# Performance work log

Hardware: AMD Instinct MI355X
Metric: run time of the kernel (lower is better)

## Reference

```python
import jax, jax.numpy as jnp
import numpy as np

B, L, H, W, C = 8, 512, 768, 12, 25
S = L * W          # span_idx count, reshaped to [B, L, W, H]
Hh = H // 2        # per-direction LSTM hidden (bidirectional)


def setup_inputs() -> dict:
    key = jax.random.key(0)
    ks = jax.random.split(key, 24)
    p = lambda k, shape: jax.random.normal(k, shape, jnp.float32) * 0.02
    z = lambda n: jnp.zeros((n,), jnp.float32)
    return {
        "we": jax.random.normal(ks[0], (B, L, H), jnp.float32),
        "mask": jnp.ones((B, L), jnp.int32),
        "span_idx": jax.random.randint(ks[1], (B, S, 2), 0, L, jnp.int32),
        "pe": jax.random.normal(ks[2], (B, C, H), jnp.float32),
        # BiLSTM params (PyTorch gate order i,f,g,o)
        "w_ih_f": p(ks[3], (4 * Hh, H)), "w_hh_f": p(ks[4], (4 * Hh, Hh)),
        "b_ih_f": z(4 * Hh), "b_hh_f": z(4 * Hh),
        "w_ih_b": p(ks[5], (4 * Hh, H)), "w_hh_b": p(ks[6], (4 * Hh, Hh)),
        "b_ih_b": z(4 * Hh), "b_hh_b": z(4 * Hh),
        # project_start MLP: H -> 4H -> H
        "start_w1": p(ks[7], (4 * H, H)), "start_b1": z(4 * H),
        "start_w2": p(ks[8], (H, 4 * H)), "start_b2": z(H),
        # project_end MLP
        "end_w1": p(ks[9], (4 * H, H)), "end_b1": z(4 * H),
        "end_w2": p(ks[10], (H, 4 * H)), "end_b2": z(H),
        # out_project MLP: 2H -> 4H -> H
        "out_w1": p(ks[11], (4 * H, 2 * H)), "out_b1": z(4 * H),
        "out_w2": p(ks[12], (H, 4 * H)), "out_b2": z(H),
        # prompt_proj MLP: H -> 4H -> H
        "pr_w1": p(ks[13], (4 * H, H)), "pr_b1": z(4 * H),
        "pr_w2": p(ks[14], (H, 4 * H)), "pr_b2": z(H),
    }


def lstm_dir(x, w_ih, w_hh, b_ih, b_hh, reverse):
    # x: [B,L,D] -> per-direction hidden sequence [B,L,Hh]
    xg = jnp.einsum('bld,gd->blg', x, w_ih) + b_ih  # precomputed input gates
    n = w_hh.shape[1]

    def step(carry, xg_t):
        h, c = carry
        g = xg_t + h @ w_hh.T + b_hh
        i, f, gg, o = jnp.split(g, 4, axis=-1)
        c = jax.nn.sigmoid(f) * c + jax.nn.sigmoid(i) * jnp.tanh(gg)
        h = jax.nn.sigmoid(o) * jnp.tanh(c)
        return (h, c), h

    init = (jnp.zeros((x.shape[0], n), x.dtype), jnp.zeros((x.shape[0], n), x.dtype))
    _, hs = jax.lax.scan(step, init, jnp.swapaxes(xg, 0, 1), reverse=reverse)
    return jnp.swapaxes(hs, 0, 1)


def mlp(x, w1, b1, w2, b2):
    # Linear -> ReLU -> (Dropout: identity in eval) -> Linear
    return jax.nn.relu(x @ w1.T + b1) @ w2.T + b2


def extract_elements(t, idx):
    # t: [B,L,D], idx: [B,S] -> [B,S,D]; indices clamped like torch
    idx = jnp.clip(idx, 0, t.shape[1] - 1)
    return jnp.take_along_axis(t, idx[..., None], axis=1)


def reference(we, mask, span_idx, pe,
              w_ih_f, w_hh_f, b_ih_f, b_hh_f,
              w_ih_b, w_hh_b, b_ih_b, b_hh_b,
              start_w1, start_b1, start_w2, start_b2,
              end_w1, end_b1, end_w2, end_b2,
              out_w1, out_b1, out_w2, out_b2,
              pr_w1, pr_b1, pr_w2, pr_b2):
    # 1) Bidirectional LSTM encoder (pad_packed zeros masked positions)
    hf = lstm_dir(we, w_ih_f, w_hh_f, b_ih_f, b_hh_f, reverse=False)
    hb = lstm_dir(we, w_ih_b, w_hh_b, b_ih_b, b_hh_b, reverse=True)
    h = jnp.concatenate([hf, hb], axis=-1) * mask[..., None].astype(we.dtype)
    # 2) SpanMarkerV0: dual MLP -> gather -> concat+relu -> out MLP
    start_rep = mlp(h, start_w1, start_b1, start_w2, start_b2)
    end_rep = mlp(h, end_w1, end_b1, end_w2, end_b2)
    ss = extract_elements(start_rep, span_idx[:, :, 0])
    es = extract_elements(end_rep, span_idx[:, :, 1])
    cat = jax.nn.relu(jnp.concatenate([ss, es], axis=-1))
    span = mlp(cat, out_w1, out_b1, out_w2, out_b2).reshape(B, L, W, H)
    # 3) Prompt projection
    prompt = mlp(pe, pr_w1, pr_b1, pr_w2, pr_b2)
    return (span, prompt)
```

## Files before the change

### kernel.cpp

```cpp
#include <hip/hip_runtime.h>
#include <hip/hip_bf16.h>
#include <stdint.h>

#define B_ 8
#define L_ 512
#define H_ 768
#define WW_ 12
#define C_ 25
#define S_ (L_*WW_)
#define HH 384
#define G4 1536

using bf16x8 = __attribute__((ext_vector_type(8))) short;
using f32x4  = __attribute__((ext_vector_type(4))) float;

static __device__ __forceinline__ unsigned short f2bf(float x){
  unsigned u = __float_as_uint(x);
  unsigned r = (u + 0x7FFFu + ((u >> 16) & 1u)) >> 16;
  return (unsigned short)r;
}
static __device__ __forceinline__ float bflo(unsigned u){ return __uint_as_float(u << 16); }
static __device__ __forceinline__ float bfhi(unsigned u){ return __uint_as_float(u & 0xFFFF0000u); }

static __device__ __forceinline__ float sigmoid_f(float x){
  x = fminf(15.f, fmaxf(-15.f, x));
  return 1.f / (1.f + __expf(-x));
}
static __device__ __forceinline__ float tanh_f(float x){
  x = fminf(15.f, fmaxf(-15.f, x));
  float e = __expf(-2.f * x);
  return (1.f - e) / (1.f + e);
}

static __device__ __forceinline__ void gl_lds16(const unsigned short* g, unsigned short* l){
  __builtin_amdgcn_global_load_lds(
      (const __attribute__((address_space(1))) unsigned int*)g,
      (__attribute__((address_space(3))) unsigned int*)l,
      16, 0, 0);
}

struct CastArgs {
  const float* s[14];
  unsigned short* d[14];
  long cum[15];
};

__global__ __launch_bounds__(256) void k_cast_multi(CastArgs a, long total){
  long i = (long)blockIdx.x * blockDim.x + threadIdx.x;
  if (i >= total) return;
  int seg = 0;
  while (i >= a.cum[seg + 1]) seg++;
  long j = i - a.cum[seg];
  float4 v = reinterpret_cast<const float4*>(a.s[seg])[j];
  ushort4 o;
  o.x = f2bf(v.x); o.y = f2bf(v.y); o.z = f2bf(v.z); o.w = f2bf(v.w);
  reinterpret_cast<ushort4*>(a.d[seg])[j] = o;
}

__global__ void k_biascomb2(const float* __restrict__ bihf, const float* __restrict__ bhhf,
                            const float* __restrict__ bihb, const float* __restrict__ bhhb,
                            float* __restrict__ o){
  int i = blockIdx.x * blockDim.x + threadIdx.x;
  if (i < 1536) o[i] = bihf[i] + bhhf[i];
  else if (i < 3072) o[i] = bihb[i - 1536] + bhhb[i - 1536];
}

template<int ACT, int OUTBF, int GX>
static __device__ __forceinline__ void gemm2_body(
    const unsigned short* __restrict__ A, const unsigned short* __restrict__ Bm,
    const float* __restrict__ bias, void* __restrict__ Cout,
    int M, int N, int K, int lda, int ldb)
{
  __shared__ unsigned short Al[128 * 64];
  __shared__ unsigned short Bl[128 * 64];

  const int tid  = threadIdx.x;
  const int lane = tid & 63;
  const int wave = tid >> 6;
  const int wr = wave >> 1, wc = wave & 1;
  const int l16 = lane & 15, lq = lane >> 4;
  const int m0 = (GX == 0 ? blockIdx.y : blockIdx.x) * 128;
  const int n0 = (GX == 0 ? blockIdx.x : blockIdx.y) * 128;

  const int r_ = tid >> 3;
  const int p_ = tid & 7;
  const int cS = ((p_ ^ (r_ & 7)) * 8);
  const unsigned short* Asrc[4];
  const unsigned short* Bsrc[4];
  #pragma unroll
  for (int i = 0; i < 4; i++){
    int ra = m0 + i * 32 + r_; ra = ra < M ? ra : (M - 1);
    Asrc[i] = A + (size_t)ra * lda + cS;
    int rb = n0 + i * 32 + r_; rb = rb < N ? rb : (N - 1);
    Bsrc[i] = Bm + (size_t)rb * ldb + cS;
  }

  f32x4 acc[4][4];
  #pragma unroll
  for (int a = 0; a < 4; a++)
    #pragma unroll
    for (int b = 0; b < 4; b++)
      acc[a][b] = (f32x4)0.f;

  const int sw0 = ((0 * 4 + lq) ^ (l16 & 7)) * 16;
  const int sw1 = ((1 * 4 + lq) ^ (l16 & 7)) * 16;
  const int aBase = (wr * 64 + l16) * 128;
  const int bBase = (wc * 64 + l16) * 128;

  for (int k0 = 0; k0 < K; k0 += 64){
    #pragma unroll
    for (int i = 0; i < 4; i++)
      gl_lds16(Asrc[i] + k0, Al + i * 2048 + tid * 8);
    #pragma unroll
    for (int i = 0; i < 4; i++)
      gl_lds16(Bsrc[i] + k0, Bl + i * 2048 + tid * 8);
    __syncthreads();

    #pragma unroll
    for (int kk = 0; kk < 2; kk++){
      const int sw = kk ? sw1 : sw0;
      bf16x8 av[4], bv[4];
      #pragma unroll
      for (int mi = 0; mi < 4; mi++)
        av[mi] = *reinterpret_cast<const bf16x8*>((const char*)Al + aBase + mi * 2048 + sw);
      #pragma unroll
      for (int ni = 0; ni < 4; ni++)
        bv[ni] = *reinterpret_cast<const bf16x8*>((const char*)Bl + bBase + ni * 2048 + sw);
      #pragma unroll
      for (int mi = 0; mi < 4; mi++)
        #pragma unroll
        for (int ni = 0; ni < 4; ni++)
          acc[mi][ni] = __builtin_amdgcn_mfma_f32_16x16x32_bf16(av[mi], bv[ni], acc[mi][ni], 0, 0, 0);
    }
    __syncthreads();
  }

  #pragma unroll
  for (int mi = 0; mi < 4; mi++){
    #pragma unroll
    for (int r = 0; r < 4; r++){
      int row = m0 + wr * 64 + mi * 16 + lq * 4 + r;
      if (row >= M) continue;
      #pragma unroll
      for (int ni = 0; ni < 4; ni++){
        int col = n0 + wc * 64 + ni * 16 + l16;
        float v = acc[mi][ni][r] + bias[col];
        if (ACT) v = v > 0.f ? v : 0.f;
        if (OUTBF) ((unsigned short*)Cout)[(size_t)row * N + col] = f2bf(v);
        else       ((float*)Cout)[(size_t)row * N + col] = v;
      }
    }
  }
}

template<int ACT, int OUTBF, int GX = 0>
__global__ __launch_bounds__(256) void k_gemm2(
    const unsigned short* A, const unsigned short* Bm,
    const float* bias, void* Cout, int M, int N, int K, int lda, int ldb)
{
  gemm2_body<ACT, OUTBF, GX>(A, Bm, bias, Cout, M, N, K, lda, ldb);
}

struct GemmPair {
  const unsigned short *A0, *A1, *B0, *B1;
  const float *b0, *b1;
  void *C0, *C1;
};

template<int ACT, int OUTBF, int GX = 0>
__global__ __launch_bounds__(256) void k_gemm2z(
    GemmPair p, int M, int N, int K, int lda, int ldb)
{
  const int z = blockIdx.z;
  gemm2_body<ACT, OUTBF, GX>(z ? p.A1 : p.A0, z ? p.B1 : p.B0,
                             z ? p.b1 : p.b0, z ? p.C1 : p.C0,
                             M, N, K, lda, ldb);
}

__global__ __launch_bounds__(512, 4) void k_gout(
    const unsigned short* __restrict__ Ps, const unsigned short* __restrict__ Pe,
    const int* __restrict__ sidx, const float* __restrict__ b1,
    const unsigned short* __restrict__ Bw, const float* __restrict__ b2,
    float* __restrict__ out)
{
  __shared__ unsigned short Al[128 * 64];
  __shared__ unsigned short Bl[256 * 64];
  __shared__ int idx2[128][2];

  const int tid  = threadIdx.x;
  const int lane = tid & 63;
  const int wave = tid >> 6;
  const int wr = wave >> 2;
  const int wc = wave & 3;
  const int l16 = lane & 15, lq = lane >> 4;

  const int wg   = blockIdx.x;
  const int xcd  = wg & 7;
  const int slot = wg >> 3;
  const int nblk = slot % 3;
  const int tm   = xcd + 8 * (slot / 3);
  const int b  = tm / 48;
  const int s0 = (tm % 48) * 128;
  const int n0 = nblk * 256;

  if (tid < 128){
    int s = s0 + tid;
    int i0 = sidx[((size_t)b * S_ + s) * 2 + 0];
    int i1 = sidx[((size_t)b * S_ + s) * 2 + 1];
    idx2[tid][0] = min(max(i0, 0), L_ - 1);
    idx2[tid][1] = min(max(i1, 0), L_ - 1);
  }
  __syncthreads();

  const int r_ = tid >> 3;
  const int p_ = tid & 7;
  const int cS = ((p_ ^ (r_ & 7)) * 8);
  const unsigned short* Bsrc[4];
  const unsigned short* As0[2];
  const unsigned short* As1[2];
  #pragma unroll
  for (int i = 0; i < 4; i++)
    Bsrc[i] = Bw + (size_t)(n0 + i * 64 + r_) * 3072 + cS;
  #pragma unroll
  for (int i = 0; i < 2; i++){
    int rr = i * 64 + r_;
    As0[i] = Ps + (size_t)(b * L_ + idx2[rr][0]) * 3072 + cS;
    As1[i] = Pe + (size_t)(b * L_ + idx2[rr][1]) * 3072 + cS;
  }

  f32x4 acc[4][4];
  #pragma unroll
  for (int a = 0; a < 4; a++)
    #pragma unroll
    for (int c = 0; c < 4; c++)
      acc[a][c] = (f32x4)0.f;

  const int sw0 = ((0 * 4 + lq) ^ (l16 & 7)) * 16;
  const int sw1 = ((1 * 4 + lq) ^ (l16 & 7)) * 16;
  const int aBase = (wr * 64 + l16) * 128;
  const int bBase = (wc * 64 + l16) * 128;

  for (int k0 = 0; k0 < 3072; k0 += 64){
    #pragma unroll
    for (int i = 0; i < 4; i++)
      gl_lds16(Bsrc[i] + k0, Bl + i * 4096 + tid * 8);
    float4 bb0 = *reinterpret_cast<const float4*>(b1 + k0 + cS);
    float4 bb1 = *reinterpret_cast<const float4*>(b1 + k0 + cS + 4);
    #pragma unroll
    for (int i = 0; i < 2; i++){
      uint4 va = *reinterpret_cast<const uint4*>(As0[i] + k0);
      uint4 ve = *reinterpret_cast<const uint4*>(As1[i] + k0);
      float f[8];
      f[0] = bflo(va.x) + bflo(ve.x) + bb0.x; f[1] = bfhi(va.x) + bfhi(ve.x) + bb0.y;
      f[2] = bflo(va.y) + bflo(ve.y) + bb0.z; f[3] = bfhi(va.y) + bfhi(ve.y) + bb0.w;
      f[4] = bflo(va.z) + bflo(ve.z) + bb1.x; f[5] = bfhi(va.z) + bfhi(ve.z) + bb1.y;
      f[6] = bflo(va.w) + bflo(ve.w) + bb1.z; f[7] = bfhi(va.w) + bfhi(ve.w) + bb1.w;
      unsigned short e[8];
      #pragma unroll
      for (int j = 0; j < 8; j++){ float v = f[j] > 0.f ? f[j] : 0.f; e[j] = f2bf(v); }
      uint4 rr;
      rr.x = (unsigned)e[0] | ((unsigned)e[1] << 16);
      rr.y = (unsigned)e[2] | ((unsigned)e[3] << 16);
      rr.z = (unsigned)e[4] | ((unsigned)e[5] << 16);
      rr.w = (unsigned)e[6] | ((unsigned)e[7] << 16);
      *reinterpret_cast<uint4*>(Al + i * 4096 + tid * 8) = rr;
    }
    __syncthreads();

    #pragma unroll
    for (int kk = 0; kk < 2; kk++){
      const int sw = kk ? sw1 : sw0;
      bf16x8 av[4], bv[4];
      #pragma unroll
      for (int mi = 0; mi < 4; mi++)
        av[mi] = *reinterpret_cast<const bf16x8*>((const char*)Al + aBase + mi * 2048 + sw);
      #pragma unroll
      for (int ni = 0; ni < 4; ni++)
        bv[ni] = *reinterpret_cast<const bf16x8*>((const char*)Bl + bBase + ni * 2048 + sw);
      #pragma unroll
      for (int mi = 0; mi < 4; mi++)
        #pragma unroll
        for (int ni = 0; ni < 4; ni++)
          acc[mi][ni] = __builtin_amdgcn_mfma_f32_16x16x32_bf16(av[mi], bv[ni], acc[mi][ni], 0, 0, 0);
    }
    __syncthreads();
  }

  #pragma unroll
  for (int mi = 0; mi < 4; mi++){
    #pragma unroll
    for (int r = 0; r < 4; r++){
      size_t row = (size_t)tm * 128 + wr * 64 + mi * 16 + lq * 4 + r;
      #pragma unroll
      for (int ni = 0; ni < 4; ni++){
        int col = n0 + wc * 64 + ni * 16 + l16;
        out[row * 768 + col] = acc[mi][ni][r] + b2[col];
      }
    }
  }
}

static __device__ __forceinline__ unsigned long long ald8(const unsigned long long* p){
  return __hip_atomic_load(p, __ATOMIC_RELAXED, __HIP_MEMORY_SCOPE_AGENT);
}

__global__ __launch_bounds__(512, 2) void k_lstm7(
    const float* __restrict__ xgc,
    const unsigned short* __restrict__ Wbf,
    const int* __restrict__ mask,
    unsigned short* __restrict__ hbf,
    unsigned int* __restrict__ hg)
{
  const int dir  = blockIdx.x / 6;
  const int part = blockIdx.x % 6;
  const int tid  = threadIdx.x;
  const int lane = tid & 63;
  const int w    = tid >> 6;
  const int l16  = lane & 15, lq = lane >> 4;

  __shared__ alignas(16) unsigned short hls[8 * HH];
  __shared__ float gsl[256 * 9];

  const float* xg = xgc + dir * 1536;
  const unsigned short* Wg = Wbf + (size_t)dir * G4 * HH;
  unsigned int* hgd = hg + dir * 2 * (8 * HH);

  bf16x8 bfr0[12], bfr1[12];
  {
    int r0 = w * 32 + l16;
    int r1 = w * 32 + 16 + l16;
    int g0 = r0 >> 6, j0u = r0 & 63;
    int g1 = r1 >> 6, j1u = r1 & 63;
    const unsigned short* p0 = Wg + ((size_t)g0 * HH + part * 64 + j0u) * HH + lq * 8;
    const unsigned short* p1 = Wg + ((size_t)g1 * HH + part * 64 + j1u) * HH + lq * 8;
    #pragma unroll
    for (int kf = 0; kf < 12; kf++){
      bfr0[kf] = *reinterpret_cast<const bf16x8*>(p0 + kf * 32);
      bfr1[kf] = *reinterpret_cast<const bf16x8*>(p1 + kf * 32);
    }
  }

  if (tid < 384) reinterpret_cast<uint4*>(hls)[tid] = uint4{0,0,0,0};

  const int cb = tid >> 6;
  const int cj = tid & 63;
  const int cu = part * 64 + cj;
  float c_state = 0.f;

  const int w0  = tid * 6;
  const int rb  = w0 / HH;
  const int ru  = w0 % HH;

  float xi, xf, xgg, xo, mvf;
  {
    const int t0 = dir ? (L_ - 1) : 0;
    const float* xr = xg + ((size_t)cb * L_ + t0) * 3072;
    xi = xr[cu]; xf = xr[HH + cu]; xgg = xr[2 * HH + cu]; xo = xr[3 * HH + cu];
    mvf = (float)mask[cb * L_ + t0];
  }

  __syncthreads();

  for (int s = 0; s < L_; s++){
    const int t = dir ? (L_ - 1 - s) : s;

    float nxi = 0.f, nxf = 0.f, nxg = 0.f, nxo = 0.f, nmv = 0.f;
    if (s + 1 < L_){
      const int tn = dir ? (L_ - 2 - s) : (s + 1);
      const float* xr = xg + ((size_t)cb * L_ + tn) * 3072;
      nxi = xr[cu]; nxf = xr[HH + cu]; nxg = xr[2 * HH + cu]; nxo = xr[3 * HH + cu];
      nmv = (float)mask[cb * L_ + tn];
    }

    if (s > 0){
      const unsigned long long tg = (unsigned long long)s;
      const unsigned long long* P =
        reinterpret_cast<const unsigned long long*>(hgd + ((s - 1) & 1) * (8 * HH) + w0);
      unsigned long long v0 = ald8(P), v1 = ald8(P + 1), v2 = ald8(P + 2);
      for (;;){
        bool ok0 = (((v0 >> 16) & 0xFFFFull) == tg) & ((v0 >> 48) == tg);
        bool ok1 = (((v1 >> 16) & 0xFFFFull) == tg) & ((v1 >> 48) == tg);
        bool ok2 = (((v2 >> 16) & 0xFFFFull) == tg) & ((v2 >> 48) == tg);
        if (ok0 & ok1 & ok2) break;
        v0 = ald8(P); v1 = ald8(P + 1); v2 = ald8(P + 2);
      }
      unsigned p01 = (unsigned)(v0 & 0xFFFFu) | ((unsigned)((v0 >> 32) & 0xFFFFu) << 16);
      unsigned p23 = (unsigned)(v1 & 0xFFFFu) | ((unsigned)((v1 >> 32) & 0xFFFFu) << 16);
      unsigned p45 = (unsigned)(v2 & 0xFFFFu) | ((unsigned)((v2 >> 32) & 0xFFFFu) << 16);
      *reinterpret_cast<unsigned*>((char*)hls + ((rb * 768 + (ru    ) * 2) ^ (rb << 4))) = p01;
      *reinterpret_cast<unsigned*>((char*)hls + ((rb * 768 + (ru + 2) * 2) ^ (rb << 4))) = p23;
      *reinterpret_cast<unsigned*>((char*)hls + ((rb * 768 + (ru + 4) * 2) ^ (rb << 4))) = p45;
    }
    __syncthreads();

    f32x4 acc0 = (f32x4)0.f, acc1 = (f32x4)0.f;
    const int arow = l16 & 7;
    #pragma unroll
    for (int kf = 0; kf < 12; kf++){
      int by = (arow * 768 + kf * 64 + lq * 16) ^ (arow << 4);
      bf16x8 a = *reinterpret_cast<const bf16x8*>((const char*)hls + by);
      acc0 = __builtin_amdgcn_mfma_f32_16x16x32_bf16(a, bfr0[kf], acc0, 0, 0, 0);
      acc1 = __builtin_amdgcn_mfma_f32_16x16x32_bf16(a, bfr1[kf], acc1, 0, 0, 0);
    }
    if (lq < 2){
      int n0r = w * 32 + l16;
      int n1r = w * 32 + 16 + l16;
      #pragma unroll
      for (int r = 0; r < 4; r++){
        gsl[n0r * 9 + lq * 4 + r] = acc0[r];
        gsl[n1r * 9 + lq * 4 + r] = acc1[r];
      }
    }
    __syncthreads();

    {
      float gi = gsl[(0 * 64 + cj) * 9 + cb] + xi;
      float gf = gsl[(1 * 64 + cj) * 9 + cb] + xf;
      float gg = gsl[(2 * 64 + cj) * 9 + cb] + xgg;
      float go = gsl[(3 * 64 + cj) * 9 + cb] + xo;
      c_state = sigmoid_f(gf) * c_state + sigmoid_f(gi) * tanh_f(gg);
      float h = sigmoid_f(go) * tanh_f(c_state);
      unsigned short hb = f2bf(h);
      *reinterpret_cast<unsigned short*>((char*)hls + ((cb * 768 + cu * 2) ^ (cb << 4))) = hb;
      unsigned word = ((unsigned)(s + 1) << 16) | (unsigned)hb;
      __hip_atomic_store(&hgd[(s & 1) * (8 * HH) + cb * HH + cu], word,
                         __ATOMIC_RELAXED, __HIP_MEMORY_SCOPE_AGENT);
      hbf[((size_t)cb * L_ + t) * H_ + dir * HH + cu] = f2bf(h * mvf);
    }

    xi = nxi; xf = nxf; xgg = nxg; xo = nxo; mvf = nmv;
  }
}

extern "C" void kernel_launch(void* const* d_in, const int* in_sizes, int n_in,
                              void* d_out, int out_size, void* d_ws, size_t ws_size,
                              hipStream_t stream)
{
  (void)in_sizes; (void)n_in; (void)out_size; (void)ws_size;
  const float* we     = (const float*)d_in[0];
  const int*   mask   = (const int*)  d_in[1];
  const int*   sidx   = (const int*)  d_in[2];
  const float* pe     = (const float*)d_in[3];
  const float* w_ih_f = (const float*)d_in[4];
  const float* w_hh_f = (const float*)d_in[5];
  const float* b_ih_f = (const float*)d_in[6];
  const float* b_hh_f = (const float*)d_in[7];
  const float* w_ih_b = (const float*)d_in[8];
  const float* w_hh_b = (const float*)d_in[9];
  const float* b_ih_b = (const float*)d_in[10];
  const float* b_hh_b = (const float*)d_in[11];
  const float* sw1 = (const float*)d_in[12]; const float* sb1 = (const float*)d_in[13];
  const float* sw2 = (const float*)d_in[14]; const float* sb2 = (const float*)d_in[15];
  const float* ew1 = (const float*)d_in[16]; const float* eb1 = (const float*)d_in[17];
  const float* ew2 = (const float*)d_in[18]; const float* eb2 = (const float*)d_in[19];
  const float* ow1 = (const float*)d_in[20]; const float* ob1 = (const float*)d_in[21];
  const float* ow2 = (const float*)d_in[22]; const float* ob2 = (const float*)d_in[23];
  const float* pw1 = (const float*)d_in[24]; const float* pb1 = (const float*)d_in[25];
  const float* pw2 = (const float*)d_in[26]; const float* pb2 = (const float*)d_in[27];

  char* wsp = (char*)d_ws; size_t off = 0;
  auto alloc = [&](size_t bytes) -> void* {
    void* p = wsp + off;
    off += (bytes + 255) & ~(size_t)255;
    return p;
  };

  unsigned short* we_bf  = (unsigned short*)alloc((size_t)4096*768*2);
  unsigned short* wihc_bf= (unsigned short*)alloc((size_t)3072*768*2);
  float* bcc   = (float*)alloc((size_t)3072*4);
  float* zerob = (float*)alloc((size_t)3072*4);
  float* sbe1  = (float*)alloc((size_t)6144*4);
  float* xgc   = (float*)alloc((size_t)4096*3072*4);
  unsigned short* whh_bf = (unsigned short*)alloc((size_t)2*1536*384*2);
  unsigned int* hg = (unsigned int*)alloc((size_t)2*2*8*384*4);
  unsigned short* h_bf  = (unsigned short*)alloc((size_t)4096*768*2);
  unsigned short* swe1b = (unsigned short*)alloc((size_t)6144*768*2);
  unsigned short* sw2b  = (unsigned short*)alloc((size_t)768*3072*2);
  unsigned short* ew2b  = (unsigned short*)alloc((size_t)768*3072*2);
  unsigned short* ow1b  = (unsigned short*)alloc((size_t)3072*1536*2);
  unsigned short* ow2b  = (unsigned short*)alloc((size_t)768*3072*2);
  unsigned short* pw1b  = (unsigned short*)alloc((size_t)3072*768*2);
  unsigned short* pw2b  = (unsigned short*)alloc((size_t)768*3072*2);
  unsigned short* srep  = (unsigned short*)alloc((size_t)4096*768*2);
  unsigned short* erep  = (unsigned short*)alloc((size_t)4096*768*2);
  unsigned short* midc  = (unsigned short*)alloc((size_t)4096*6144*2);
  unsigned short* pe_bf = (unsigned short*)alloc((size_t)200*768*2);
  unsigned short* pmid  = (unsigned short*)alloc((size_t)200*3072*2);

  unsigned short* Ps = (unsigned short*)xgc;
  unsigned short* Pe = (unsigned short*)xgc + (size_t)4096*3072;

  hipMemsetAsync(hg, 0, (size_t)2*2*8*384*4, stream);
  hipMemsetAsync(zerob, 0, (size_t)3072*4, stream);
  hipMemcpyAsync(sbe1,        sb1, (size_t)3072*4, hipMemcpyDeviceToDevice, stream);
  hipMemcpyAsync(sbe1 + 3072, eb1, (size_t)3072*4, hipMemcpyDeviceToDevice, stream);

  {
    CastArgs ca;
    const float* srcs[14] = { we, w_ih_f, w_ih_b, w_hh_f, w_hh_b, sw1, ew1,
                              sw2, ew2, ow1, ow2, pw1, pw2, pe };
    unsigned short* dsts[14] = { we_bf, wihc_bf, wihc_bf + 1536*768,
                                 whh_bf, whh_bf + 1536*384,
                                 swe1b, swe1b + 3072*768,
                                 sw2b, ew2b, ow1b, ow2b, pw1b, pw2b, pe_bf };
    long n4s[14] = { 4096L*768/4, 1536L*768/4, 1536L*768/4,
                     1536L*384/4, 1536L*384/4,
                     3072L*768/4, 3072L*768/4,
                     768L*3072/4, 768L*3072/4, 3072L*1536/4, 768L*3072/4,
                     3072L*768/4, 768L*3072/4, 200L*768/4 };
    long c = 0;
    for (int i = 0; i < 14; i++){ ca.s[i] = srcs[i]; ca.d[i] = dsts[i]; ca.cum[i] = c; c += n4s[i]; }
    ca.cum[14] = c;
    int grid = (int)((c + 255) / 256);
    k_cast_multi<<<grid, 256, 0, stream>>>(ca, c);
  }

  k_biascomb2<<<12, 256, 0, stream>>>(b_ih_f, b_hh_f, b_ih_b, b_hh_b, bcc);

  dim3 blk(256);
  k_gemm2<0,0><<<dim3(24, 32), blk, 0, stream>>>(we_bf, wihc_bf, bcc, xgc, 4096, 3072, 768, 768, 768);

  k_lstm7<<<12, 512, 0, stream>>>(xgc, whh_bf, mask, h_bf, hg);

  k_gemm2<1,1><<<dim3(48, 32), blk, 0, stream>>>(h_bf, swe1b, sbe1, midc, 4096, 6144, 768, 768, 768);

  {
    GemmPair p;
    p.A0 = midc;        p.B0 = sw2b; p.b0 = sb2; p.C0 = srep;
    p.A1 = midc + 3072; p.B1 = ew2b; p.b1 = eb2; p.C1 = erep;
    k_gemm2z<1,1,1><<<dim3(32, 6, 2), blk, 0, stream>>>(p, 4096, 768, 3072, 6144, 3072);
  }

  {
    GemmPair p;
    p.A0 = srep; p.B0 = ow1b;       p.b0 = zerob; p.C0 = Ps;
    p.A1 = erep; p.B1 = ow1b + 768; p.b1 = zerob; p.C1 = Pe;
    k_gemm2z<0,1,0><<<dim3(24, 32, 2), blk, 0, stream>>>(p, 4096, 3072, 768, 768, 1536);
  }

  float* outp = (float*)d_out;
  k_gout<<<1152, dim3(512), 0, stream>>>(Ps, Pe, sidx, ob1, ow2b, ob2, outp);

  k_gemm2<1,1><<<dim3(24, 2), blk, 0, stream>>>(pe_bf, pw1b, pb1, pmid, 200, 3072, 768, 768, 768);
  k_gemm2<0,0><<<dim3( 6, 2), blk, 0, stream>>>(pmid, pw2b, pb2,
                                                outp + (size_t)37748736, 200, 768, 3072, 3072, 3072);
}
```

Before: 1.683 ms.

## Fuse LSTM and downstream MLP GEMMs into one persistent kernel with progress flags

Combines the sequential LSTM kernel with the start/end MLP GEMMs, the out_project first layer and the prompt first layer into a single launch. Blocks wait on atomic progress counters: the LSTM publishes every 64 timesteps, and GEMM tiles for row blocks whose hidden states are already complete start while the recurrence is still running. This is meant to fill idle CUs during the latency-bound LSTM and to remove several launch boundaries. In exchange it depends on the LSTM blocks being resident before the waiting blocks, which they are given by being the lowest block ids, and it uses a new 128x256 tile GEMM with 512 threads.

```diff
diff --git a/kernel.cpp b/kernel.cpp
--- a/kernel.cpp
+++ b/kernel.cpp
@@ -37,6 +37,10 @@
       (const __attribute__((address_space(1))) unsigned int*)g,
       (__attribute__((address_space(3))) unsigned int*)l,
       16, 0, 0);
+}
+
+static __device__ __forceinline__ int aload(const int* p){
+  return __hip_atomic_load(p, __ATOMIC_ACQUIRE, __HIP_MEMORY_SCOPE_AGENT);
 }
 
 struct CastArgs {
@@ -65,8 +69,8 @@
   else if (i < 3072) o[i] = bihb[i - 1536] + bhhb[i - 1536];
 }
 
-template<int ACT, int OUTBF, int GX>
-static __device__ __forceinline__ void gemm2_body(
+template<int ACT, int OUTBF>
+__global__ __launch_bounds__(256) void k_gemm2(
     const unsigned short* __restrict__ A, const unsigned short* __restrict__ Bm,
     const float* __restrict__ bias, void* __restrict__ Cout,
     int M, int N, int K, int lda, int ldb)
@@ -79,8 +83,8 @@
   const int wave = tid >> 6;
   const int wr = wave >> 1, wc = wave & 1;
   const int l16 = lane & 15, lq = lane >> 4;
-  const int m0 = (GX == 0 ? blockIdx.y : blockIdx.x) * 128;
-  const int n0 = (GX == 0 ? blockIdx.x : blockIdx.y) * 128;
+  const int m0 = blockIdx.y * 128;
+  const int n0 = blockIdx.x * 128;
 
   const int r_ = tid >> 3;
   const int p_ = tid & 7;
@@ -153,79 +157,33 @@
   }
 }
 
-template<int ACT, int OUTBF, int GX = 0>
-__global__ __launch_bounds__(256) void k_gemm2(
-    const unsigned short* A, const unsigned short* Bm,
-    const float* bias, void* Cout, int M, int N, int K, int lda, int ldb)
+static __device__ void gemm512(
+    const unsigned short* __restrict__ A, const unsigned short* __restrict__ Bm,
+    const float* __restrict__ bias, unsigned short* __restrict__ C,
+    int M, int N, int K, int lda, int ldb, int m0, int n0, int act, char* ldsraw)
 {
-  gemm2_body<ACT, OUTBF, GX>(A, Bm, bias, Cout, M, N, K, lda, ldb);
-}
-
-struct GemmPair {
-  const unsigned short *A0, *A1, *B0, *B1;
-  const float *b0, *b1;
-  void *C0, *C1;
-};
-
-template<int ACT, int OUTBF, int GX = 0>
-__global__ __launch_bounds__(256) void k_gemm2z(
-    GemmPair p, int M, int N, int K, int lda, int ldb)
-{
-  const int z = blockIdx.z;
-  gemm2_body<ACT, OUTBF, GX>(z ? p.A1 : p.A0, z ? p.B1 : p.B0,
-                             z ? p.b1 : p.b0, z ? p.C1 : p.C0,
-                             M, N, K, lda, ldb);
-}
-
-__global__ __launch_bounds__(512, 4) void k_gout(
-    const unsigned short* __restrict__ Ps, const unsigned short* __restrict__ Pe,
-    const int* __restrict__ sidx, const float* __restrict__ b1,
-    const unsigned short* __restrict__ Bw, const float* __restrict__ b2,
-    float* __restrict__ out)
-{
-  __shared__ unsigned short Al[128 * 64];
-  __shared__ unsigned short Bl[256 * 64];
-  __shared__ int idx2[128][2];
-
+  unsigned short* Al = (unsigned short*)ldsraw;
+  unsigned short* Bl = (unsigned short*)(ldsraw + 16384);
   const int tid  = threadIdx.x;
   const int lane = tid & 63;
   const int wave = tid >> 6;
-  const int wr = wave >> 2;
-  const int wc = wave & 3;
+  const int wr = wave >> 2, wc = wave & 3;
   const int l16 = lane & 15, lq = lane >> 4;
-
-  const int wg   = blockIdx.x;
-  const int xcd  = wg & 7;
-  const int slot = wg >> 3;
-  const int nblk = slot % 3;
-  const int tm   = xcd + 8 * (slot / 3);
-  const int b  = tm / 48;
-  const int s0 = (tm % 48) * 128;
-  const int n0 = nblk * 256;
-
-  if (tid < 128){
-    int s = s0 + tid;
-    int i0 = sidx[((size_t)b * S_ + s) * 2 + 0];
-    int i1 = sidx[((size_t)b * S_ + s) * 2 + 1];
-    idx2[tid][0] = min(max(i0, 0), L_ - 1);
-    idx2[tid][1] = min(max(i1, 0), L_ - 1);
-  }
-  __syncthreads();
-
   const int r_ = tid >> 3;
   const int p_ = tid & 7;
   const int cS = ((p_ ^ (r_ & 7)) * 8);
+
+  const unsigned short* Asrc[2];
   const unsigned short* Bsrc[4];
-  const unsigned short* As0[2];
-  const unsigned short* As1[2];
-  #pragma unroll
-  for (int i = 0; i < 4; i++)
-    Bsrc[i] = Bw + (size_t)(n0 + i * 64 + r_) * 3072 + cS;
   #pragma unroll
   for (int i = 0; i < 2; i++){
-    int rr = i * 64 + r_;
-    As0[i] = Ps + (size_t)(b * L_ + idx2[rr][0]) * 3072 + cS;
-    As1[i] = Pe + (size_t)(b * L_ + idx2[rr][1]) * 3072 + cS;
+    int ra = m0 + i * 64 + r_; ra = ra < M ? ra : (M - 1);
+    Asrc[i] = A + (size_t)ra * lda + cS;
+  }
+  #pragma unroll
+  for (int i = 0; i < 4; i++){
+    int rb = n0 + i * 64 + r_; rb = rb < N ? rb : (N - 1);
+    Bsrc[i] = Bm + (size_t)rb * ldb + cS;
   }
 
   f32x4 acc[4][4];
@@ -240,31 +198,13 @@
   const int aBase = (wr * 64 + l16) * 128;
   const int bBase = (wc * 64 + l16) * 128;
 
-  for (int k0 = 0; k0 < 3072; k0 += 64){
+  for (int k0 = 0; k0 < K; k0 += 64){
+    #pragma unroll
+    for (int i = 0; i < 2; i++)
+      gl_lds16(Asrc[i] + k0, Al + i * 4096 + tid * 8);
     #pragma unroll
     for (int i = 0; i < 4; i++)
       gl_lds16(Bsrc[i] + k0, Bl + i * 4096 + tid * 8);
-    float4 bb0 = *reinterpret_cast<const float4*>(b1 + k0 + cS);
-    float4 bb1 = *reinterpret_cast<const float4*>(b1 + k0 + cS + 4);
-    #pragma unroll
-    for (int i = 0; i < 2; i++){
-      uint4 va = *reinterpret_cast<const uint4*>(As0[i] + k0);
-      uint4 ve = *reinterpret_cast<const uint4*>(As1[i] + k0);
-      float f[8];
-      f[0] = bflo(va.x) + bflo(ve.x) + bb0.x; f[1] = bfhi(va.x) + bfhi(ve.x) + bb0.y;
-      f[2] = bflo(va.y) + bflo(ve.y) + bb0.z; f[3] = bfhi(va.y) + bfhi(ve.y) + bb0.w;
-      f[4] = bflo(va.z) + bflo(ve.z) + bb1.x; f[5] = bfhi(va.z) + bfhi(ve.z) + bb1.y;
-      f[6] = bflo(va.w) + bflo(ve.w) + bb1.z; f[7] = bfhi(va.w) + bfhi(ve.w) + bb1.w;
-      unsigned short e[8];
-      #pragma unroll
-      for (int j = 0; j < 8; j++){ float v = f[j] > 0.f ? f[j] : 0.f; e[j] = f2bf(v); }
-      uint4 rr;
-      rr.x = (unsigned)e[0] | ((unsigned)e[1] << 16);
-      rr.y = (unsigned)e[2] | ((unsigned)e[3] << 16);
-      rr.z = (unsigned)e[4] | ((unsigned)e[5] << 16);
-      rr.w = (unsigned)e[6] | ((unsigned)e[7] << 16);
-      *reinterpret_cast<uint4*>(Al + i * 4096 + tid * 8) = rr;
-    }
     __syncthreads();
 
     #pragma unroll
@@ -290,11 +230,14 @@
   for (int mi = 0; mi < 4; mi++){
     #pragma unroll
     for (int r = 0; r < 4; r++){
-      size_t row = (size_t)tm * 128 + wr * 64 + mi * 16 + lq * 4 + r;
+      int row = m0 + wr * 64 + mi * 16 + lq * 4 + r;
+      if (row >= M) continue;
       #pragma unroll
       for (int ni = 0; ni < 4; ni++){
         int col = n0 + wc * 64 + ni * 16 + l16;
-        out[row * 768 + col] = acc[mi][ni][r] + b2[col];
+        float v = acc[mi][ni][r] + bias[col];
+        if (act) v = v > 0.f ? v : 0.f;
+        C[(size_t)row * N + col] = f2bf(v);
       }
     }
   }
@@ -304,22 +247,23 @@
   return __hip_atomic_load(p, __ATOMIC_RELAXED, __HIP_MEMORY_SCOPE_AGENT);
 }
 
-__global__ __launch_bounds__(512, 2) void k_lstm7(
-    const float* __restrict__ xgc,
-    const unsigned short* __restrict__ Wbf,
-    const int* __restrict__ mask,
-    unsigned short* __restrict__ hbf,
-    unsigned int* __restrict__ hg)
+static __device__ void lstm_body(
+    int bid, const float* __restrict__ xgc,
+    const unsigned short* __restrict__ Wbf, const int* __restrict__ mask,
+    unsigned short* __restrict__ hbf, unsigned int* __restrict__ hg,
+    int* __restrict__ prog, char* ldsraw)
 {
-  const int dir  = blockIdx.x / 6;
-  const int part = blockIdx.x % 6;
+  __builtin_amdgcn_s_setprio(1);
+
+  const int dir  = bid / 6;
+  const int part = bid % 6;
   const int tid  = threadIdx.x;
   const int lane = tid & 63;
   const int w    = tid >> 6;
   const int l16  = lane & 15, lq = lane >> 4;
 
-  __shared__ alignas(16) unsigned short hls[8 * HH];
-  __shared__ float gsl[256 * 9];
+  unsigned short* hls = (unsigned short*)ldsraw;
+  float* gsl = (float*)(ldsraw + 8192);
 
   const float* xg = xgc + dir * 1536;
   const unsigned short* Wg = Wbf + (size_t)dir * G4 * HH;
@@ -428,7 +372,232 @@
       hbf[((size_t)cb * L_ + t) * H_ + dir * HH + cu] = f2bf(h * mvf);
     }
 
+    if ((s & 63) == 63){
+      __threadfence();
+      __syncthreads();
+      if (tid == 0)
+        __hip_atomic_store(&prog[dir * 6 + part], (s >> 6) + 1,
+                           __ATOMIC_RELEASE, __HIP_MEMORY_SCOPE_AGENT);
+    }
+
     xi = nxi; xf = nxf; xgg = nxg; xo = nxo; mvf = nmv;
+  }
+}
+
+__global__ __launch_bounds__(512, 2) void k_mega(
+    const float* __restrict__ xgc, const unsigned short* __restrict__ whh_bf,
+    const int* __restrict__ mask, unsigned short* __restrict__ h_bf,
+    unsigned int* __restrict__ hg,
+    int* __restrict__ prog, int* __restrict__ aCnt, int* __restrict__ bCnt,
+    const unsigned short* __restrict__ swe1b, const float* __restrict__ sbe1,
+    unsigned short* __restrict__ midc,
+    const unsigned short* __restrict__ sw2b, const unsigned short* __restrict__ ew2b,
+    const float* __restrict__ sb2, const float* __restrict__ eb2,
+    unsigned short* __restrict__ srep, unsigned short* __restrict__ erep,
+    const unsigned short* __restrict__ ow1b, const float* __restrict__ zerob,
+    unsigned short* __restrict__ Ps, unsigned short* __restrict__ Pe,
+    const unsigned short* __restrict__ pe_bf, const unsigned short* __restrict__ pw1b,
+    const float* __restrict__ pb1, unsigned short* __restrict__ pmid)
+{
+  __shared__ char ldsraw[49152];
+
+  int bid = blockIdx.x;
+  if (bid < 12){
+    lstm_body(bid, xgc, whh_bf, mask, h_bf, hg, prog, ldsraw);
+    return;
+  }
+  bid -= 12;
+
+  const unsigned short *A, *Bm; const float* bias; unsigned short* C;
+  int M = 4096, N, K, lda, ldb, m0, n0, act;
+  const int* pollPtr = nullptr; int pollTarget = 0;
+  int lstmM = -1;
+  int* pubPtr = nullptr;
+
+  if (bid < 384 || (bid >= 864 && bid < 1248)){
+    int inner = bid < 384;
+    int u = inner ? bid : bid - 864;
+    int q = u / 24, n = u % 24;
+    int m = inner ? ((q >> 1) * 4 + 1 + (q & 1)) : ((q >> 1) * 4 + 3 * (q & 1));
+    lstmM = m;
+    A = h_bf; lda = 768; Bm = swe1b; ldb = 768; bias = sbe1;
+    C = midc; N = 6144; K = 768; m0 = m * 128; n0 = n * 256; act = 1;
+    pubPtr = &aCnt[m];
+  } else if ((bid >= 384 && bid < 480) || (bid >= 1248 && bid < 1344)){
+    int inner = bid < 480;
+    int u = inner ? bid - 384 : bid - 1248;
+    int q = u / 6, r = u % 6, z = r / 3, n = r % 3;
+    int m = inner ? ((q >> 1) * 4 + 1 + (q & 1)) : ((q >> 1) * 4 + 3 * (q & 1));
+    A = midc + z * 3072; lda = 6144;
+    Bm = z ? ew2b : sw2b; ldb = 3072;
+    bias = z ? eb2 : sb2;
+    C = z ? erep : srep; N = 768; K = 3072; m0 = m * 128; n0 = n * 256; act = 1;
+    pollPtr = &aCnt[m]; pollTarget = 24;
+    pubPtr = &bCnt[m * 2 + z];
+  } else if ((bid >= 480 && bid < 864) || (bid >= 1344 && bid < 1728)){
+    int inner = bid < 864;
+    int u = inner ? bid - 480 : bid - 1344;
+    int q = u / 24, r = u % 24, z = r / 12, n = r % 12;
+    int m = inner ? ((q >> 1) * 4 + 1 + (q & 1)) : ((q >> 1) * 4 + 3 * (q & 1));
+    A = z ? erep : srep; lda = 768;
+    Bm = ow1b + z * 768; ldb = 1536;
+    bias = zerob;
+    C = z ? Pe : Ps; N = 3072; K = 768; m0 = m * 128; n0 = n * 256; act = 0;
+    pollPtr = &bCnt[m * 2 + z]; pollTarget = 3;
+  } else {
+    int u = bid - 1728;
+    A = pe_bf; lda = 768; Bm = pw1b; ldb = 768; bias = pb1;
+    C = pmid; M = 200; N = 3072; K = 768;
+    m0 = (u / 12) * 128; n0 = (u % 12) * 256; act = 1;
+  }
+
+  if (lstmM >= 0){
+    const int cf = (lstmM & 3) * 2 + 2;
+    const int cbk = 8 - (lstmM & 3) * 2;
+    for (;;){
+      bool ok = true;
+      #pragma unroll
+      for (int p = 0; p < 6; p++){
+        ok &= (aload(&prog[p])     >= cf);
+        ok &= (aload(&prog[6 + p]) >= cbk);
+      }
+      if (ok) break;
+      __builtin_amdgcn_s_sleep(8);
+    }
+  } else if (pollPtr){
+    while (aload(pollPtr) < pollTarget) __builtin_amdgcn_s_sleep(8);
+  }
+
+  gemm512(A, Bm, bias, C, M, N, K, lda, ldb, m0, n0, act, ldsraw);
+
+  if (pubPtr){
+    __threadfence();
+    __syncthreads();
+    if (threadIdx.x == 0)
+      __hip_atomic_fetch_add(pubPtr, 1, __ATOMIC_RELEASE, __HIP_MEMORY_SCOPE_AGENT);
+  }
+}
+
+__global__ __launch_bounds__(512, 4) void k_gout(
+    const unsigned short* __restrict__ Ps, const unsigned short* __restrict__ Pe,
+    const int* __restrict__ sidx, const float* __restrict__ b1,
+    const unsigned short* __restrict__ Bw, const float* __restrict__ b2,
+    float* __restrict__ out)
+{
+  __shared__ unsigned short Al[128 * 64];
+  __shared__ unsigned short Bl[256 * 64];
+  __shared__ int idx2[128][2];
+
+  const int tid  = threadIdx.x;
+  const int lane = tid & 63;
+  const int wave = tid >> 6;
+  const int wr = wave >> 2;
+  const int wc = wave & 3;
+  const int l16 = lane & 15, lq = lane >> 4;
+
+  const int wg   = blockIdx.x;
+  const int xcd  = wg & 7;
+  const int slot = wg >> 3;
+  const int nblk = slot % 3;
+  const int tm   = xcd + 8 * (slot / 3);
+  const int b  = tm / 48;
+  const int s0 = (tm % 48) * 128;
+  const int n0 = nblk * 256;
+
+  if (tid < 128){
+    int s = s0 + tid;
+    int i0 = sidx[((size_t)b * S_ + s) * 2 + 0];
+    int i1 = sidx[((size_t)b * S_ + s) * 2 + 1];
+    idx2[tid][0] = min(max(i0, 0), L_ - 1);
+    idx2[tid][1] = min(max(i1, 0), L_ - 1);
+  }
+  __syncthreads();
+
+  const int r_ = tid >> 3;
+  const int p_ = tid & 7;
+  const int cS = ((p_ ^ (r_ & 7)) * 8);
+  const unsigned short* Bsrc[4];
+  const unsigned short* As0[2];
+  const unsigned short* As1[2];
+  #pragma unroll
+  for (int i = 0; i < 4; i++)
+    Bsrc[i] = Bw + (size_t)(n0 + i * 64 + r_) * 3072 + cS;
+  #pragma unroll
+  for (int i = 0; i < 2; i++){
+    int rr = i * 64 + r_;
+    As0[i] = Ps + (size_t)(b * L_ + idx2[rr][0]) * 3072 + cS;
+    As1[i] = Pe + (size_t)(b * L_ + idx2[rr][1]) * 3072 + cS;
+  }
+
+  f32x4 acc[4][4];
+  #pragma unroll
+  for (int a = 0; a < 4; a++)
+    #pragma unroll
+    for (int c = 0; c < 4; c++)
+      acc[a][c] = (f32x4)0.f;
+
+  const int sw0 = ((0 * 4 + lq) ^ (l16 & 7)) * 16;
+  const int sw1 = ((1 * 4 + lq) ^ (l16 & 7)) * 16;
+  const int aBase = (wr * 64 + l16) * 128;
+  const int bBase = (wc * 64 + l16) * 128;
+
+  for (int k0 = 0; k0 < 3072; k0 += 64){
+    #pragma unroll
+    for (int i = 0; i < 4; i++)
+      gl_lds16(Bsrc[i] + k0, Bl + i * 4096 + tid * 8);
+    float4 bb0 = *reinterpret_cast<const float4*>(b1 + k0 + cS);
+    float4 bb1 = *reinterpret_cast<const float4*>(b1 + k0 + cS + 4);
+    #pragma unroll
+    for (int i = 0; i < 2; i++){
+      uint4 va = *reinterpret_cast<const uint4*>(As0[i] + k0);
+      uint4 ve = *reinterpret_cast<const uint4*>(As1[i] + k0);
+      float f[8];
+      f[0] = bflo(va.x) + bflo(ve.x) + bb0.x; f[1] = bfhi(va.x) + bfhi(ve.x) + bb0.y;
+      f[2] = bflo(va.y) + bflo(ve.y) + bb0.z; f[3] = bfhi(va.y) + bfhi(ve.y) + bb0.w;
+      f[4] = bflo(va.z) + bflo(ve.z) + bb1.x; f[5] = bfhi(va.z) + bfhi(ve.z) + bb1.y;
+      f[6] = bflo(va.w) + bflo(ve.w) + bb1.z; f[7] = bfhi(va.w) + bfhi(ve.w) + bb1.w;
+      unsigned short e[8];
+      #pragma unroll
+      for (int j = 0; j < 8; j++){ float v = f[j] > 0.f ? f[j] : 0.f; e[j] = f2bf(v); }
+      uint4 rr;
+      rr.x = (unsigned)e[0] | ((unsigned)e[1] << 16);
+      rr.y = (unsigned)e[2] | ((unsigned)e[3] << 16);
+      rr.z = (unsigned)e[4] | ((unsigned)e[5] << 16);
+      rr.w = (unsigned)e[6] | ((unsigned)e[7] << 16);
+      *reinterpret_cast<uint4*>(Al + i * 4096 + tid * 8) = rr;
+    }
+    __syncthreads();
+
+    #pragma unroll
+    for (int kk = 0; kk < 2; kk++){
+      const int sw = kk ? sw1 : sw0;
+      bf16x8 av[4], bv[4];
+      #pragma unroll
+      for (int mi = 0; mi < 4; mi++)
+        av[mi] = *reinterpret_cast<const bf16x8*>((const char*)Al + aBase + mi * 2048 + sw);
+      #pragma unroll
+      for (int ni = 0; ni < 4; ni++)
+        bv[ni] = *reinterpret_cast<const bf16x8*>((const char*)Bl + bBase + ni * 2048 + sw);
+      #pragma unroll
+      for (int mi = 0; mi < 4; mi++)
+        #pragma unroll
+        for (int ni = 0; ni < 4; ni++)
+          acc[mi][ni] = __builtin_amdgcn_mfma_f32_16x16x32_bf16(av[mi], bv[ni], acc[mi][ni], 0, 0, 0);
+    }
+    __syncthreads();
+  }
+
+  #pragma unroll
+  for (int mi = 0; mi < 4; mi++){
+    #pragma unroll
+    for (int r = 0; r < 4; r++){
+      size_t row = (size_t)tm * 128 + wr * 64 + mi * 16 + lq * 4 + r;
+      #pragma unroll
+      for (int ni = 0; ni < 4; ni++){
+        int col = n0 + wc * 64 + ni * 16 + l16;
+        out[row * 768 + col] = acc[mi][ni][r] + b2[col];
+      }
+    }
   }
 }
 
@@ -473,6 +642,7 @@
   float* xgc   = (float*)alloc((size_t)4096*3072*4);
   unsigned short* whh_bf = (unsigned short*)alloc((size_t)2*1536*384*2);
   unsigned int* hg = (unsigned int*)alloc((size_t)2*2*8*384*4);
+  int* flags = (int*)alloc(128*4);
   unsigned short* h_bf  = (unsigned short*)alloc((size_t)4096*768*2);
   unsigned short* swe1b = (unsigned short*)alloc((size_t)6144*768*2);
   unsigned short* sw2b  = (unsigned short*)alloc((size_t)768*3072*2);
@@ -489,8 +659,12 @@
 
   unsigned short* Ps = (unsigned short*)xgc;
   unsigned short* Pe = (unsigned short*)xgc + (size_t)4096*3072;
+  int* prog = flags;
+  int* aCnt = flags + 16;
+  int* bCnt = flags + 48;
 
   hipMemsetAsync(hg, 0, (size_t)2*2*8*384*4, stream);
+  hipMemsetAsync(flags, 0, 128*4, stream);
   hipMemsetAsync(zerob, 0, (size_t)3072*4, stream);
   hipMemcpyAsync(sbe1,        sb1, (size_t)3072*4, hipMemcpyDeviceToDevice, stream);
   hipMemcpyAsync(sbe1 + 3072, eb1, (size_t)3072*4, hipMemcpyDeviceToDevice, stream);
@@ -520,28 +694,14 @@
   dim3 blk(256);
   k_gemm2<0,0><<<dim3(24, 32), blk, 0, stream>>>(we_bf, wihc_bf, bcc, xgc, 4096, 3072, 768, 768, 768);
 
-  k_lstm7<<<12, 512, 0, stream>>>(xgc, whh_bf, mask, h_bf, hg);
-
-  k_gemm2<1,1><<<dim3(48, 32), blk, 0, stream>>>(h_bf, swe1b, sbe1, midc, 4096, 6144, 768, 768, 768);
-
-  {
-    GemmPair p;
-    p.A0 = midc;        p.B0 = sw2b; p.b0 = sb2; p.C0 = srep;
-    p.A1 = midc + 3072; p.B1 = ew2b; p.b1 = eb2; p.C1 = erep;
-    k_gemm2z<1,1,1><<<dim3(32, 6, 2), blk, 0, stream>>>(p, 4096, 768, 3072, 6144, 3072);
-  }
-
-  {
-    GemmPair p;
-    p.A0 = srep; p.B0 = ow1b;       p.b0 = zerob; p.C0 = Ps;
-    p.A1 = erep; p.B1 = ow1b + 768; p.b1 = zerob; p.C1 = Pe;
-    k_gemm2z<0,1,0><<<dim3(24, 32, 2), blk, 0, stream>>>(p, 4096, 3072, 768, 768, 1536);
-  }
+  k_mega<<<1764, dim3(512), 0, stream>>>(
+      xgc, whh_bf, mask, h_bf, hg, prog, aCnt, bCnt,
+      swe1b, sbe1, midc, sw2b, ew2b, sb2, eb2, srep, erep,
+      ow1b, zerob, Ps, Pe, pe_bf, pw1b, pb1, pmid);
 
   float* outp = (float*)d_out;
   k_gout<<<1152, dim3(512), 0, stream>>>(Ps, Pe, sidx, ob1, ow2b, ob2, outp);
 
-  k_gemm2<1,1><<<dim3(24, 2), blk, 0, stream>>>(pe_bf, pw1b, pb1, pmid, 200, 3072, 768, 768, 768);
-  k_gemm2<0,0><<<dim3( 6, 2), blk, 0, stream>>>(pmid, pw2b, pb2,
-                                                outp + (size_t)37748736, 200, 768, 3072, 3072, 3072);
-}
+  k_gemm2<0,0><<<dim3(6, 2), blk, 0, stream>>>(pmid, pw2b, pb2,
+                                               outp + (size_t)37748736, 200, 768, 3072, 3072, 3072);
+}
```

Result: slower. 5.151 ms, median of 2 (+206.0%).
